# Kernel optimization log

Hardware: AMD Instinct MI355X
Metric: run time of the kernel (lower is better)

The kernel has to match this reference:

```python
import jax, jax.numpy as jnp
import numpy as np
import math

B, S, D, H = 4, 2048, 1024, 16
DK = D // H

def setup_inputs() -> dict:
    key = jax.random.key(0)
    ks = jax.random.split(key, 12)
    scale = 1.0 / math.sqrt(D)
    inp = {
        "query": jax.random.normal(ks[0], (B, S, D), jnp.float32),
        "key_": jax.random.normal(ks[1], (B, S, D), jnp.float32),
        "value": jax.random.normal(ks[2], (B, S, D), jnp.float32),
        "mask": jnp.broadcast_to(jnp.tril(jnp.ones((S, S), jnp.int32)), (B, S, S)),
        "Wq": jax.random.normal(ks[3], (D, D), jnp.float32) * scale,
        "bq": jnp.zeros((D,), jnp.float32),
        "Wk": jax.random.normal(ks[4], (D, D), jnp.float32) * scale,
        "bk": jnp.zeros((D,), jnp.float32),
        "Wv": jax.random.normal(ks[5], (D, D), jnp.float32) * scale,
        "bv": jnp.zeros((D,), jnp.float32),
        "Wo": jax.random.normal(ks[6], (D, D), jnp.float32) * scale,
        "bo": jnp.zeros((D,), jnp.float32),
    }
    return inp

def reference(query, key_, value, mask, Wq, bq, Wk, bk, Wv, bv, Wo, bo):
    # Linear projections (torch Linear: x @ W^T + b), split into heads [B,H,S,DK]
    def proj(x, W, b):
        y = jnp.einsum('bsd,ed->bse', x, W) + b
        return y.reshape(B, S, H, DK).transpose(0, 2, 1, 3)
    Q = proj(query, Wq, bq)
    K = proj(key_, Wk, bk)
    V = proj(value, Wv, bv)
    # scaled dot-product attention with additive mask-fill
    scores = jnp.einsum('bhqd,bhkd->bhqk', Q, K) / math.sqrt(DK)
    scores = jnp.where(mask[:, None, :, :] == 0, jnp.float32(-1e9), scores)
    attn = jax.nn.softmax(scores, axis=-1)  # dropout p=0.0 (eval) -> identity
    ctx = jnp.einsum('bhqk,bhkd->bhqd', attn, V)
    ctx = ctx.transpose(0, 2, 1, 3).reshape(B, S, D)
    out = jnp.einsum('bsd,ed->bse', ctx, Wo) + bo
    return out
```

## Files before the change

kernel.cpp:

```cpp
#include <hip/hip_runtime.h>
#include <hip/hip_bf16.h>
#include <cstdint>
#include <cstddef>

static constexpr int kB = 4, kS = 2048, kD = 1024, kH = 16, kDK = 64;
static constexpr int kM = kB * kS;

typedef __attribute__((ext_vector_type(8))) __bf16 bf16x8;
typedef __attribute__((ext_vector_type(4))) __bf16 bf16x4;
typedef __attribute__((ext_vector_type(4))) float f32x4;

#define MFMA_BF16(a, b, c) __builtin_amdgcn_mfma_f32_16x16x32_bf16((a), (b), (c), 0, 0, 0)

#define GLDS16(gp, lp)                                                        \
  __builtin_amdgcn_global_load_lds(                                           \
      (__attribute__((address_space(1))) void*)(gp),                          \
      (__attribute__((address_space(3))) void*)(lp), 16, 0, 0)

__device__ __forceinline__ bf16x8 cvt8(const float* s, int i) {
  const float4 a = ((const float4*)s)[i * 2 + 0];
  const float4 b = ((const float4*)s)[i * 2 + 1];
  bf16x8 o;
  o[0] = (__bf16)a.x; o[1] = (__bf16)a.y; o[2] = (__bf16)a.z; o[3] = (__bf16)a.w;
  o[4] = (__bf16)b.x; o[5] = (__bf16)b.y; o[6] = (__bf16)b.z; o[7] = (__bf16)b.w;
  return o;
}

__global__ __launch_bounds__(256) void cvt_f32_bf16(
    const float* __restrict__ src, __bf16* __restrict__ dst, int n8) {
  const int i = blockIdx.x * 256 + threadIdx.x;
  if (i >= n8) return;
  ((bf16x8*)dst)[i] = cvt8(src, i);
}

__global__ __launch_bounds__(256) void cvt_all(
    const float* __restrict__ q, const float* __restrict__ k,
    const float* __restrict__ v, const float* __restrict__ wq,
    const float* __restrict__ wk, const float* __restrict__ wv,
    const float* __restrict__ wo, __bf16* __restrict__ dq,
    __bf16* __restrict__ dk, __bf16* __restrict__ dv,
    __bf16* __restrict__ dwq, __bf16* __restrict__ dwk,
    __bf16* __restrict__ dwv, __bf16* __restrict__ dwo) {
  int bid = blockIdx.x;
  const float* s;
  __bf16* d;
  int i;
  if (bid < 3 * 4096) {
    const int seg = bid >> 12;
    i = (bid & 4095) * 256 + threadIdx.x;
    s = seg == 0 ? q : seg == 1 ? k : v;
    d = seg == 0 ? dq : seg == 1 ? dk : dv;
  } else {
    bid -= 3 * 4096;
    const int seg = bid >> 9;
    i = (bid & 511) * 256 + threadIdx.x;
    s = seg == 0 ? wq : seg == 1 ? wk : seg == 2 ? wv : wo;
    d = seg == 0 ? dwq : seg == 1 ? dwk : seg == 2 ? dwv : dwo;
  }
  ((bf16x8*)d)[i] = cvt8(s, i);
}

template <int MT, typename OutT>
__device__ __forceinline__ void gemm_core(
    const __bf16* __restrict__ A, const __bf16* __restrict__ W,
    const float* __restrict__ bias, OutT* __restrict__ out, int mode, int bid,
    __bf16* As, __bf16* Ws) {
  constexpr int RT = MT / 32;
  constexpr int AISS = MT / 32;
  constexpr int MTILES = 8192 / MT;
  const int tid = threadIdx.x;
  const int wave = tid >> 6, lane = tid & 63;
  const int col = lane & 15, quad = lane >> 4;
  const int m0 = (bid % MTILES) * MT;
  const int n0 = (bid / MTILES) * 128;
  const int wr = (wave & 1) * (MT / 2);
  const int wc = (wave >> 1) * 64;

  f32x4 acc[RT][4] = {};

  const int g0f = ((quad) ^ (col & 7)) * 16;
  const int g1f = ((quad + 4) ^ (col & 7)) * 16;

  for (int k0 = 0; k0 < 1024; k0 += 64) {
#pragma unroll
    for (int i = 0; i < AISS; ++i) {
      const int s = i * 256 + tid;
      GLDS16(A + (size_t)(m0 + (s >> 3)) * 1024 + k0 +
                 (((s & 7) ^ ((s >> 3) & 7)) * 8),
             (char*)As + i * 4096 + wave * 1024);
    }
#pragma unroll
    for (int i = 0; i < 4; ++i) {
      const int s = i * 256 + tid;
      GLDS16(W + (size_t)(n0 + (s >> 3)) * 1024 + k0 +
                 (((s & 7) ^ ((s >> 3) & 7)) * 8),
             (char*)Ws + i * 4096 + wave * 1024);
    }
    __syncthreads();
#pragma unroll
    for (int h = 0; h < 2; ++h) {
      const int go = h ? g1f : g0f;
      bf16x8 af[RT], wf[4];
#pragma unroll
      for (int t = 0; t < RT; ++t)
        af[t] = *(const bf16x8*)((const char*)As + (wr + t * 16 + col) * 128 + go);
#pragma unroll
      for (int t = 0; t < 4; ++t)
        wf[t] = *(const bf16x8*)((const char*)Ws + (wc + t * 16 + col) * 128 + go);
#pragma unroll
      for (int rt = 0; rt < RT; ++rt)
#pragma unroll
        for (int ct = 0; ct < 4; ++ct)
          acc[rt][ct] = MFMA_BF16(af[rt], wf[ct], acc[rt][ct]);
    }
    __syncthreads();
  }

#pragma unroll
  for (int ct = 0; ct < 4; ++ct) {
    const int n = n0 + wc + ct * 16 + col;
    const float bb = bias[n];
#pragma unroll
    for (int rt = 0; rt < RT; ++rt) {
#pragma unroll
      for (int r = 0; r < 4; ++r) {
        const int m = m0 + wr + rt * 16 + quad * 4 + r;
        const float v = acc[rt][ct][r] + bb;
        size_t idx;
        if (mode == 0) {
          idx = (size_t)m * 1024 + n;
        } else {
          const int b = m >> 11, s = m & 2047;
          const int h2 = n >> 6, dk = n & 63;
          if (mode == 1)
            idx = ((size_t)(b * 16 + h2) * 2048 + s) * 64 + dk;
          else
            idx = ((size_t)(b * 16 + h2) * 64 + dk) * 2048 + s;
        }
        out[idx] = (OutT)v;
      }
    }
  }
}

template <int MODE, int MT, typename OutT>
__global__ __launch_bounds__(256) void gemm_one(
    const __bf16* __restrict__ A, const __bf16* __restrict__ W,
    const float* __restrict__ bias, OutT* __restrict__ out) {
  __shared__ __align__(16) __bf16 As[MT * 64];
  __shared__ __align__(16) __bf16 Ws[128 * 64];
  gemm_core<MT, OutT>(A, W, bias, out, MODE, blockIdx.x, As, Ws);
}

__global__ __launch_bounds__(256) void gemm_qkv(
    const __bf16* __restrict__ Aq, const __bf16* __restrict__ Ak,
    const __bf16* __restrict__ Av, const __bf16* __restrict__ Wqb,
    const __bf16* __restrict__ Wkb, const __bf16* __restrict__ Wvb,
    const float* __restrict__ bq, const float* __restrict__ bk,
    const float* __restrict__ bv, __bf16* __restrict__ Qw,
    __bf16* __restrict__ Kw, __bf16* __restrict__ Vw) {
  __shared__ __align__(16) __bf16 As[128 * 64];
  __shared__ __align__(16) __bf16 Ws[128 * 64];
  const int seg = blockIdx.x >> 9;
  const int bid = blockIdx.x & 511;
  const __bf16* A = seg == 0 ? Aq : seg == 1 ? Ak : Av;
  const __bf16* W = seg == 0 ? Wqb : seg == 1 ? Wkb : Wvb;
  const float* bias = seg == 0 ? bq : seg == 1 ? bk : bv;
  __bf16* out = seg == 0 ? Qw : seg == 1 ? Kw : Vw;
  gemm_core<128, __bf16>(A, W, bias, out, seg == 2 ? 2 : 1, bid, As, Ws);
}

__global__ __launch_bounds__(256, 4) void flash_attn(
    const __bf16* __restrict__ Q, const __bf16* __restrict__ K,
    const __bf16* __restrict__ Vt, __bf16* __restrict__ ctx) {
  __shared__ __align__(16) __bf16 Ks[2][64 * 64];
  __shared__ __align__(16) __bf16 Vs[2][64 * 64];

  const int tid = threadIdx.x;
  const int wave = tid >> 6, lane = tid & 63;
  const int col = lane & 15, quad = lane >> 4;
  const int bh = blockIdx.x >> 4;
  const int pair = blockIdx.x & 15;
  const int b = bh >> 4, h = bh & 15;
  const int t_lo = pair, t_hi = 31 - pair;
  const int q0f[2] = {t_lo * 64 + wave * 16, t_hi * 64 + wave * 16};

  constexpr float SCL = 0.18033688011112042f;

  bf16x8 qf[2][2];
#pragma unroll
  for (int f = 0; f < 2; ++f) {
    const __bf16* Qp = Q + ((size_t)bh * kS + q0f[f] + col) * 64 + quad * 8;
    qf[f][0] = *(const bf16x8*)Qp;
    qf[f][1] = *(const bf16x8*)(Qp + 32);
  }

  f32x4 o[2][4] = {};
  float lsum[2] = {0.f, 0.f};

  const __bf16* Kg = K + (size_t)bh * kS * 64;
  const __bf16* Vg = Vt + (size_t)bh * 64 * kS;

  const int row0 = tid >> 3;
  const int g0 = ((tid & 7) ^ (row0 & 7)) * 8;
  const int ksrc0 = (row0 & ~12) | ((row0 & 4) << 1) | ((row0 & 8) >> 1);

  auto stage = [&](int c, int buf) {
    const int k0 = c * 64;
    char* KB = (char*)Ks[buf] + wave * 1024;
    char* VB = (char*)Vs[buf] + wave * 1024;
    GLDS16(Kg + (size_t)(k0 + ksrc0) * 64 + g0, KB);
    GLDS16(Vg + (size_t)row0 * kS + k0 + g0, VB);
    GLDS16(Kg + (size_t)(k0 + ksrc0 + 32) * 64 + g0, KB + 4096);
    GLDS16(Vg + (size_t)(row0 + 32) * kS + k0 + g0, VB + 4096);
  };

  const int kq0 = ((quad) ^ (col & 7)) * 16;
  const int kq1 = ((quad + 4) ^ (col & 7)) * 16;

  stage(0, 0);

  for (int c = 0; c <= t_hi; ++c) {
    __syncthreads();
    if (c < t_hi) stage(c + 1, (c + 1) & 1);
    const bool lo = (c <= t_lo);
    const bool d0 = (c == t_lo), d1 = (c == t_hi);
    const int k0 = c * 64;
    const char* KB = (const char*)Ks[c & 1];
    const char* VB = (const char*)Vs[c & 1];

    bf16x8 pb[2][2];
#pragma unroll
    for (int kt = 0; kt < 4; ++kt) {
      const int krow = (col & 7) | ((kt & 1) << 3) | ((col & 8) << 1) |
                       ((kt >> 1) << 5);
      const bf16x8 kf0 = *(const bf16x8*)(KB + krow * 128 + kq0);
      const bf16x8 kf1 = *(const bf16x8*)(KB + krow * 128 + kq1);
      f32x4 z = {};
      const f32x4 s1 = MFMA_BF16(kf1, qf[1][1], MFMA_BF16(kf0, qf[1][0], z));
      f32x4 s0 = z;
      if (lo) s0 = MFMA_BF16(kf1, qf[0][1], MFMA_BF16(kf0, qf[0][0], z));
      const int kbase = k0 + (kt >> 1) * 32 + quad * 8 + (kt & 1) * 4;
#pragma unroll
      for (int r = 0; r < 4; ++r) {
        float e1 = __builtin_amdgcn_exp2f(s1[r] * SCL);
        if (d1 && (kbase + r > q0f[1] + col)) e1 = 0.0f;
        lsum[1] += e1;
        pb[1][kt >> 1][(kt & 1) * 4 + r] = (__bf16)e1;
        float e0 = __builtin_amdgcn_exp2f(s0[r] * SCL);
        if (d0 && (kbase + r > q0f[0] + col)) e0 = 0.0f;
        if (lo) lsum[0] += e0;
        pb[0][kt >> 1][(kt & 1) * 4 + r] = (__bf16)e0;
      }
    }
#pragma unroll
    for (int dt = 0; dt < 4; ++dt) {
      const char* vp = VB + (dt * 16 + col) * 128;
      const bf16x8 vf0 = *(const bf16x8*)(vp + kq0);
      const bf16x8 vf1 = *(const bf16x8*)(vp + kq1);
      o[1][dt] = MFMA_BF16(vf1, pb[1][1], MFMA_BF16(vf0, pb[1][0], o[1][dt]));
      if (lo) o[0][dt] = MFMA_BF16(vf1, pb[0][1], MFMA_BF16(vf0, pb[0][0], o[0][dt]));
    }
  }

#pragma unroll
  for (int f = 0; f < 2; ++f) {
    float l = lsum[f];
    l += __shfl_xor(l, 16, 64);
    l += __shfl_xor(l, 32, 64);
    const float inv = 1.0f / l;
    __bf16* cp = ctx + ((size_t)b * kS + q0f[f] + col) * kD + h * 64 + quad * 4;
#pragma unroll
    for (int dt = 0; dt < 4; ++dt) {
      bf16x4 w;
#pragma unroll
      for (int r = 0; r < 4; ++r) w[r] = (__bf16)(o[f][dt][r] * inv);
      *(bf16x4*)(cp + dt * 16) = w;
    }
  }
}

extern "C" void kernel_launch(void* const* d_in, const int* in_sizes, int n_in,
                              void* d_out, int out_size, void* d_ws, size_t ws_size,
                              hipStream_t stream) {
  const float* query = (const float*)d_in[0];
  const float* key_  = (const float*)d_in[1];
  const float* value = (const float*)d_in[2];
  const float* Wq = (const float*)d_in[4];
  const float* bq = (const float*)d_in[5];
  const float* Wk = (const float*)d_in[6];
  const float* bk = (const float*)d_in[7];
  const float* Wv = (const float*)d_in[8];
  const float* bv = (const float*)d_in[9];
  const float* Wo = (const float*)d_in[10];
  const float* bo = (const float*)d_in[11];

  const size_t e = (size_t)kM * kD;
  const size_t w = (size_t)kD * kD;
  float* out = (float*)d_out;

  const size_t REQ = (6 * e + 4 * w) * sizeof(__bf16);

  if (ws_size >= REQ) {
    __bf16* Qw  = (__bf16*)d_ws;
    __bf16* Kw  = Qw + e;
    __bf16* Vw  = Kw + e;
    __bf16* Aq  = Vw + e;
    __bf16* Ak  = Aq + e;
    __bf16* Av  = Ak + e;
    __bf16* Wqb = Av + e;
    __bf16* Wkb = Wqb + w;
    __bf16* Wvb = Wkb + w;
    __bf16* Wob = Wvb + w;

    cvt_all<<<3 * 4096 + 4 * 512, 256, 0, stream>>>(
        query, key_, value, Wq, Wk, Wv, Wo, Aq, Ak, Av, Wqb, Wkb, Wvb, Wob);
    gemm_qkv<<<1536, 256, 0, stream>>>(Aq, Ak, Av, Wqb, Wkb, Wvb, bq, bk, bv,
                                       Qw, Kw, Vw);
    flash_attn<<<kB * kH * 16, 256, 0, stream>>>(Qw, Kw, Vw, Aq);
    gemm_one<0, 64, float><<<1024, 256, 0, stream>>>(Aq, Wob, bo, out);
  } else {
    __bf16* Qw = (__bf16*)d_ws;
    __bf16* Kw = Qw + e;
    __bf16* Vw = Kw + e;
    __bf16* Ab = Vw + e;
    __bf16* Wb = Ab + e;

    const int actg = (int)(e / 8 / 256);
    const int wg = (int)(w / 8 / 256);
    cvt_f32_bf16<<<actg, 256, 0, stream>>>(query, Ab, (int)(e / 8));
    cvt_f32_bf16<<<wg, 256, 0, stream>>>(Wq, Wb, (int)(w / 8));
    gemm_one<1, 128, __bf16><<<512, 256, 0, stream>>>(Ab, Wb, bq, Qw);
    cvt_f32_bf16<<<actg, 256, 0, stream>>>(key_, Ab, (int)(e / 8));
    cvt_f32_bf16<<<wg, 256, 0, stream>>>(Wk, Wb, (int)(w / 8));
    gemm_one<1, 128, __bf16><<<512, 256, 0, stream>>>(Ab, Wb, bk, Kw);
    cvt_f32_bf16<<<actg, 256, 0, stream>>>(value, Ab, (int)(e / 8));
    cvt_f32_bf16<<<wg, 256, 0, stream>>>(Wv, Wb, (int)(w / 8));
    gemm_one<2, 128, __bf16><<<512, 256, 0, stream>>>(Ab, Wb, bv, Vw);
    flash_attn<<<kB * kH * 16, 256, 0, stream>>>(Qw, Kw, Vw, Ab);
    cvt_f32_bf16<<<wg, 256, 0, stream>>>(Wo, Wb, (int)(w / 8));
    gemm_one<0, 64, float><<<1024, 256, 0, stream>>>(Ab, Wb, bo, out);
  }
}
```

Before: 363.9 us.

## Double-buffer GEMM shared-memory tiles with K=32 stages and prefetch

Rewrites the GEMM core to use two shared-memory buffers, each holding a 128x32 A slice and a 128x32 W slice packed together. The loads for the next K-step are issued before the current step's MFMAs, which removes one barrier per iteration and overlaps global-to-LDS traffic with compute. The output projection now uses 128x128 tiles (512 blocks) instead of 64-row tiles, giving fewer blocks and higher register pressure for that GEMM.

```diff
diff --git a/kernel.cpp b/kernel.cpp
--- a/kernel.cpp
+++ b/kernel.cpp
@@ -60,60 +60,56 @@
   ((bf16x8*)d)[i] = cvt8(s, i);
 }
 
-template <int MT, typename OutT>
+template <typename OutT>
 __device__ __forceinline__ void gemm_core(
     const __bf16* __restrict__ A, const __bf16* __restrict__ W,
     const float* __restrict__ bias, OutT* __restrict__ out, int mode, int bid,
-    __bf16* As, __bf16* Ws) {
-  constexpr int RT = MT / 32;
-  constexpr int AISS = MT / 32;
-  constexpr int MTILES = 8192 / MT;
+    __bf16* Sm ) {
   const int tid = threadIdx.x;
   const int wave = tid >> 6, lane = tid & 63;
   const int col = lane & 15, quad = lane >> 4;
-  const int m0 = (bid % MTILES) * MT;
-  const int n0 = (bid / MTILES) * 128;
-  const int wr = (wave & 1) * (MT / 2);
-  const int wc = (wave >> 1) * 64;
-
-  f32x4 acc[RT][4] = {};
-
-  const int g0f = ((quad) ^ (col & 7)) * 16;
-  const int g1f = ((quad + 4) ^ (col & 7)) * 16;
-
-  for (int k0 = 0; k0 < 1024; k0 += 64) {
-#pragma unroll
-    for (int i = 0; i < AISS; ++i) {
-      const int s = i * 256 + tid;
-      GLDS16(A + (size_t)(m0 + (s >> 3)) * 1024 + k0 +
-                 (((s & 7) ^ ((s >> 3) & 7)) * 8),
-             (char*)As + i * 4096 + wave * 1024);
-    }
-#pragma unroll
-    for (int i = 0; i < 4; ++i) {
-      const int s = i * 256 + tid;
-      GLDS16(W + (size_t)(n0 + (s >> 3)) * 1024 + k0 +
-                 (((s & 7) ^ ((s >> 3) & 7)) * 8),
-             (char*)Ws + i * 4096 + wave * 1024);
-    }
+  const int m0 = (bid & 63) * 128;
+  const int n0 = (bid >> 6) * 128;
+  const int wr = (wave & 1) * 64, wc = (wave >> 1) * 64;
+
+  f32x4 acc[4][4] = {};
+
+  const __bf16* srcs[4];
+#pragma unroll
+  for (int i = 0; i < 4; ++i) {
+    const int row = i * 32 + (tid >> 3);
+    const int gg = (tid & 7) ^ (row & 7);
+    srcs[i] = (gg < 4) ? A + (size_t)(m0 + row) * 1024 + gg * 8
+                       : W + (size_t)(n0 + row) * 1024 + (gg - 4) * 8;
+  }
+
+  auto stage = [&](int k0, int buf) {
+    char* base = (char*)Sm + buf * 16384 + wave * 1024;
+#pragma unroll
+    for (int i = 0; i < 4; ++i) GLDS16(srcs[i] + k0, base + i * 4096);
+  };
+
+  const int ga = ((quad) ^ (col & 7)) * 16;
+  const int gw = ((quad + 4) ^ (col & 7)) * 16;
+
+  stage(0, 0);
+
+#pragma unroll 2
+  for (int k = 0; k < 32; ++k) {
     __syncthreads();
-#pragma unroll
-    for (int h = 0; h < 2; ++h) {
-      const int go = h ? g1f : g0f;
-      bf16x8 af[RT], wf[4];
-#pragma unroll
-      for (int t = 0; t < RT; ++t)
-        af[t] = *(const bf16x8*)((const char*)As + (wr + t * 16 + col) * 128 + go);
-#pragma unroll
-      for (int t = 0; t < 4; ++t)
-        wf[t] = *(const bf16x8*)((const char*)Ws + (wc + t * 16 + col) * 128 + go);
-#pragma unroll
-      for (int rt = 0; rt < RT; ++rt)
-#pragma unroll
-        for (int ct = 0; ct < 4; ++ct)
-          acc[rt][ct] = MFMA_BF16(af[rt], wf[ct], acc[rt][ct]);
-    }
-    __syncthreads();
+    if (k < 31) stage((k + 1) * 32, (k + 1) & 1);
+    const char* Bp = (const char*)Sm + (k & 1) * 16384;
+    bf16x8 af[4], wf[4];
+#pragma unroll
+    for (int t = 0; t < 4; ++t) {
+      af[t] = *(const bf16x8*)(Bp + (wr + t * 16 + col) * 128 + ga);
+      wf[t] = *(const bf16x8*)(Bp + (wc + t * 16 + col) * 128 + gw);
+    }
+#pragma unroll
+    for (int rt = 0; rt < 4; ++rt)
+#pragma unroll
+      for (int ct = 0; ct < 4; ++ct)
+        acc[rt][ct] = MFMA_BF16(af[rt], wf[ct], acc[rt][ct]);
   }
 
 #pragma unroll
@@ -121,7 +117,7 @@
     const int n = n0 + wc + ct * 16 + col;
     const float bb = bias[n];
 #pragma unroll
-    for (int rt = 0; rt < RT; ++rt) {
+    for (int rt = 0; rt < 4; ++rt) {
 #pragma unroll
       for (int r = 0; r < 4; ++r) {
         const int m = m0 + wr + rt * 16 + quad * 4 + r;
@@ -143,13 +139,12 @@
   }
 }
 
-template <int MODE, int MT, typename OutT>
+template <int MODE, typename OutT>
 __global__ __launch_bounds__(256) void gemm_one(
     const __bf16* __restrict__ A, const __bf16* __restrict__ W,
     const float* __restrict__ bias, OutT* __restrict__ out) {
-  __shared__ __align__(16) __bf16 As[MT * 64];
-  __shared__ __align__(16) __bf16 Ws[128 * 64];
-  gemm_core<MT, OutT>(A, W, bias, out, MODE, blockIdx.x, As, Ws);
+  __shared__ __align__(16) __bf16 Sm[2][128 * 64];
+  gemm_core<OutT>(A, W, bias, out, MODE, blockIdx.x, &Sm[0][0]);
 }
 
 __global__ __launch_bounds__(256) void gemm_qkv(
@@ -159,15 +154,14 @@
     const float* __restrict__ bq, const float* __restrict__ bk,
     const float* __restrict__ bv, __bf16* __restrict__ Qw,
     __bf16* __restrict__ Kw, __bf16* __restrict__ Vw) {
-  __shared__ __align__(16) __bf16 As[128 * 64];
-  __shared__ __align__(16) __bf16 Ws[128 * 64];
+  __shared__ __align__(16) __bf16 Sm[2][128 * 64];
   const int seg = blockIdx.x >> 9;
   const int bid = blockIdx.x & 511;
   const __bf16* A = seg == 0 ? Aq : seg == 1 ? Ak : Av;
   const __bf16* W = seg == 0 ? Wqb : seg == 1 ? Wkb : Wvb;
   const float* bias = seg == 0 ? bq : seg == 1 ? bk : bv;
   __bf16* out = seg == 0 ? Qw : seg == 1 ? Kw : Vw;
-  gemm_core<128, __bf16>(A, W, bias, out, seg == 2 ? 2 : 1, bid, As, Ws);
+  gemm_core<__bf16>(A, W, bias, out, seg == 2 ? 2 : 1, bid, &Sm[0][0]);
 }
 
 __global__ __launch_bounds__(256, 4) void flash_attn(
@@ -318,7 +312,7 @@
     gemm_qkv<<<1536, 256, 0, stream>>>(Aq, Ak, Av, Wqb, Wkb, Wvb, bq, bk, bv,
                                        Qw, Kw, Vw);
     flash_attn<<<kB * kH * 16, 256, 0, stream>>>(Qw, Kw, Vw, Aq);
-    gemm_one<0, 64, float><<<1024, 256, 0, stream>>>(Aq, Wob, bo, out);
+    gemm_one<0, float><<<512, 256, 0, stream>>>(Aq, Wob, bo, out);
   } else {
     __bf16* Qw = (__bf16*)d_ws;
     __bf16* Kw = Qw + e;
@@ -330,15 +324,15 @@
     const int wg = (int)(w / 8 / 256);
     cvt_f32_bf16<<<actg, 256, 0, stream>>>(query, Ab, (int)(e / 8));
     cvt_f32_bf16<<<wg, 256, 0, stream>>>(Wq, Wb, (int)(w / 8));
-    gemm_one<1, 128, __bf16><<<512, 256, 0, stream>>>(Ab, Wb, bq, Qw);
+    gemm_one<1, __bf16><<<512, 256, 0, stream>>>(Ab, Wb, bq, Qw);
     cvt_f32_bf16<<<actg, 256, 0, stream>>>(key_, Ab, (int)(e / 8));
     cvt_f32_bf16<<<wg, 256, 0, stream>>>(Wk, Wb, (int)(w / 8));
-    gemm_one<1, 128, __bf16><<<512, 256, 0, stream>>>(Ab, Wb, bk, Kw);
+    gemm_one<1, __bf16><<<512, 256, 0, stream>>>(Ab, Wb, bk, Kw);
     cvt_f32_bf16<<<actg, 256, 0, stream>>>(value, Ab, (int)(e / 8));
     cvt_f32_bf16<<<wg, 256, 0, stream>>>(Wv, Wb, (int)(w / 8));
-    gemm_one<2, 128, __bf16><<<512, 256, 0, stream>>>(Ab, Wb, bv, Vw);
+    gemm_one<2, __bf16><<<512, 256, 0, stream>>>(Ab, Wb, bv, Vw);
     flash_attn<<<kB * kH * 16, 256, 0, stream>>>(Qw, Kw, Vw, Ab);
     cvt_f32_bf16<<<wg, 256, 0, stream>>>(Wo, Wb, (int)(w / 8));
-    gemm_one<0, 64, float><<<1024, 256, 0, stream>>>(Ab, Wb, bo, out);
-  }
-}
+    gemm_one<0, float><<<512, 256, 0, stream>>>(Ab, Wb, bo, out);
+  }
+}
```

New measurement: 364.4 us. No clear change (+0.2%).
